# Optimization experiments

Measured on AMD Instinct MI355X. Metric: run time of the kernel, lower is better.

The kernel has to match this reference:

```python
import jax, jax.numpy as jnp
import numpy as np

N, E, D = 50000, 800000, 128
EPS = 1e-5


def _layernorm(x, g, b):
    m = jnp.mean(x, axis=-1, keepdims=True)
    v = jnp.mean((x - m) ** 2, axis=-1, keepdims=True)
    return (x - m) * jax.lax.rsqrt(v + EPS) * g + b


def setup_inputs() -> dict:
    key = jax.random.key(0)
    ks = jax.random.split(key, 8)
    x = jax.random.normal(ks[0], (N, D), dtype=jnp.float32)
    edge_index = jax.random.randint(ks[1], (2, E), 0, N, dtype=jnp.int64)
    edge_weights = jax.random.uniform(ks[2], (E,), dtype=jnp.float32)
    s = 1.0 / np.sqrt(D)
    W1 = jax.random.uniform(ks[3], (D, D), minval=-s, maxval=s, dtype=jnp.float32)
    b1 = jax.random.uniform(ks[4], (D,), minval=-s, maxval=s, dtype=jnp.float32)
    W2 = jax.random.uniform(ks[5], (D, D), minval=-s, maxval=s, dtype=jnp.float32)
    b2 = jax.random.uniform(ks[6], (D,), minval=-s, maxval=s, dtype=jnp.float32)
    g1 = jnp.ones((D,), jnp.float32); be1 = jnp.zeros((D,), jnp.float32)
    g2 = jnp.ones((D,), jnp.float32); be2 = jnp.zeros((D,), jnp.float32)
    return {"x": x, "edge_index": edge_index, "edge_weights": edge_weights,
            "W1": W1, "b1": b1, "g1": g1, "be1": be1,
            "W2": W2, "b2": b2, "g2": g2, "be2": be2}


def _layer(x, src, dst, ew, W, b, g, be):
    h = jax.nn.relu(x @ W + b)                      # [N, D]
    msg = ew[:, None] * h[src]                      # [E, D] gather
    h = h + jax.ops.segment_sum(msg, dst, num_segments=N)  # scatter-add (matches serial loop)
    return _layernorm(h, g, be)                     # dropout is identity at inference


def reference(x, edge_index, edge_weights, W1, b1, g1, be1, W2, b2, g2, be2):
    src, dst = edge_index[0], edge_index[1]
    x = _layer(x, src, dst, edge_weights, W1, b1, g1, be1)
    x = _layer(x, src, dst, edge_weights, W2, b2, g2, be2)
    return x
```

## Files before the change

### kernel.cpp

```cpp
#include <hip/hip_runtime.h>
#include <hip/hip_bf16.h>


#define D 128
#define SA 8192

typedef __attribute__((ext_vector_type(8))) short short8;
typedef __attribute__((ext_vector_type(4))) float f32x4;
typedef __attribute__((ext_vector_type(2))) unsigned int uint2v;
typedef __attribute__((ext_vector_type(4))) unsigned int uint4v;

__global__ __launch_bounds__(256) void k_prep(const float* __restrict__ W1,
                                              const float* __restrict__ W2,
                                              short* __restrict__ WT1,
                                              short* __restrict__ WT2,
                                              int* __restrict__ bhist, int nb) {
    int b = blockIdx.x;
    if (b < 128) {
        const float* W = (b < 64) ? W1 : W2;
        short* WT = (b < 64) ? WT1 : WT2;
        int i = (b & 63) * 256 + threadIdx.x;
        int k = i >> 7, nn = i & 127;
        WT[nn * 128 + k] = (short)__bfloat16_as_ushort(__float2bfloat16(W[i]));
    } else {
        for (int i = threadIdx.x; i < nb; i += 256) bhist[i] = 0;
    }
}

__global__ __launch_bounds__(1024) void k_bhist(const int* __restrict__ dst, int e,
                                                int n, int nb,
                                                int* __restrict__ bhist) {
    __shared__ int lh[784];
    int tid = threadIdx.x;
    for (int i = tid; i < nb; i += 1024) lh[i] = 0;
    __syncthreads();
    int i0 = blockIdx.x * SA;
#pragma unroll
    for (int k = 0; k < SA / 1024; ++k) {
        int i = i0 + k * 1024 + tid;
        if (i < e) {
            int d = dst[i];
            d = min(max(d, 0), n - 1);
            atomicAdd(&lh[d >> 6], 1);
        }
    }
    __syncthreads();
    for (int i = tid; i < nb; i += 1024)
        if (lh[i]) atomicAdd(&bhist[i], lh[i]);
}

__global__ __launch_bounds__(1024) void k_bscan(const int* __restrict__ bhist, int nb,
                                                int* __restrict__ boff,
                                                int* __restrict__ bcursor) {
    __shared__ int s[1024];
    int t = threadIdx.x;
    int v = (t < nb) ? bhist[t] : 0;
    s[t] = v;
    __syncthreads();
    for (int off = 1; off < 1024; off <<= 1) {
        int u = (t >= off) ? s[t - off] : 0;
        __syncthreads();
        s[t] += u;
        __syncthreads();
    }
    if (t < nb) {
        int ex = s[t] - v;
        boff[t] = ex;
        bcursor[t] = ex;
    }
}

__global__ __launch_bounds__(1024) void k_bfill(const int* __restrict__ src,
                                                const int* __restrict__ dst,
                                                const float* __restrict__ ew, int e,
                                                int n, int nb,
                                                int* __restrict__ bcursor,
                                                uint2v* __restrict__ csr_tmp) {
    __shared__ int lh[784];
    __shared__ int gbase[784];
    int tid = threadIdx.x;
    for (int i = tid; i < nb; i += 1024) lh[i] = 0;
    __syncthreads();
    int i0 = blockIdx.x * SA;
    int bkt[SA / 1024], pos[SA / 1024];
    unsigned pk[SA / 1024];
    float wv[SA / 1024];
#pragma unroll
    for (int k = 0; k < SA / 1024; ++k) {
        int i = i0 + k * 1024 + tid;
        bkt[k] = -1;
        if (i < e) {
            int d = dst[i];
            d = min(max(d, 0), n - 1);
            int s = src[i];
            s = min(max(s, 0), n - 1);
            int b = d >> 6;
            bkt[k] = b;
            pos[k] = atomicAdd(&lh[b], 1);
            pk[k] = (unsigned)s | ((unsigned)(d & 63) << 16);
            wv[k] = ew[i];
        }
    }
    __syncthreads();
    for (int i = tid; i < nb; i += 1024)
        gbase[i] = lh[i] ? atomicAdd(&bcursor[i], lh[i]) : 0;
    __syncthreads();
#pragma unroll
    for (int k = 0; k < SA / 1024; ++k) {
        if (bkt[k] >= 0) {
            int idx = gbase[bkt[k]] + pos[k];
            uint2v en;
            en.x = pk[k];
            en.y = __float_as_uint(wv[k]);
            csr_tmp[idx] = en;
        }
    }
}

#define STG 3072
__global__ __launch_bounds__(256) void k_bfinal(const uint2v* __restrict__ csr_tmp,
                                                const int* __restrict__ boff, int n,
                                                int e, int nb,
                                                int* __restrict__ row_ptr,
                                                uint2v* __restrict__ csr) {
    __shared__ uint2v stage[STG];
    __shared__ int dh[64], dcur[64], dscan[64];
    int b = blockIdx.x;
    int tid = threadIdx.x;
    int base = boff[b];
    int endo = (b + 1 < nb) ? boff[b + 1] : e;
    int cnt = endo - base;
    int ndst = min(64, n - b * 64);
    bool st = (cnt <= STG);
    if (tid < 64) { dh[tid] = 0; dcur[tid] = 0; }
    __syncthreads();
    for (int i = tid; i < cnt; i += 256) {
        uint2v en = csr_tmp[base + i];
        if (st) stage[i] = en;
        atomicAdd(&dh[(en.x >> 16) & 63], 1);
    }
    __syncthreads();
    if (tid < 64) {
        int v = dh[tid];
        int incl = v;
#pragma unroll
        for (int off = 1; off < 64; off <<= 1) {
            int u = __shfl_up(incl, off, 64);
            if (tid >= off) incl += u;
        }
        dscan[tid] = incl - v;
        if (tid < ndst) row_ptr[b * 64 + tid] = base + incl - v;
        if (b == nb - 1 && tid == 0) row_ptr[n] = e;
    }
    __syncthreads();
    for (int i = tid; i < cnt; i += 256) {
        uint2v en = st ? stage[i] : csr_tmp[base + i];
        int dlo = (en.x >> 16) & 63;
        int p = atomicAdd(&dcur[dlo], 1);
        csr[base + dscan[dlo] + p] = en;
    }
}

__device__ __forceinline__ short8 cvt8v(f32x4 lo, f32x4 hi) {
    short8 r;
    r[0] = (short)__bfloat16_as_ushort(__float2bfloat16(lo.x));
    r[1] = (short)__bfloat16_as_ushort(__float2bfloat16(lo.y));
    r[2] = (short)__bfloat16_as_ushort(__float2bfloat16(lo.z));
    r[3] = (short)__bfloat16_as_ushort(__float2bfloat16(lo.w));
    r[4] = (short)__bfloat16_as_ushort(__float2bfloat16(hi.x));
    r[5] = (short)__bfloat16_as_ushort(__float2bfloat16(hi.y));
    r[6] = (short)__bfloat16_as_ushort(__float2bfloat16(hi.z));
    r[7] = (short)__bfloat16_as_ushort(__float2bfloat16(hi.w));
    return r;
}

template <int F32IN>
__global__ __launch_bounds__(256) void k_gemm_mfma(const float* __restrict__ xf,
                                                   const short* __restrict__ xb,
                                                   const short* __restrict__ WT,
                                                   const float* __restrict__ bias,
                                                   ushort* __restrict__ hb, int n) {
    int lane = threadIdx.x & 63;
    int w = threadIdx.x >> 6;
    int ln = lane & 15, g = lane >> 4;
    int nt0 = w, nt1 = w + 4;
    short8 bfr0[4], bfr1[4];
#pragma unroll
    for (int kk = 0; kk < 4; ++kk) {
        bfr0[kk] = *(const short8*)(WT + (nt0 * 16 + ln) * 128 + kk * 32 + g * 8);
        bfr1[kk] = *(const short8*)(WT + (nt1 * 16 + ln) * 128 + kk * 32 + g * 8);
    }
    float bv0 = bias[nt0 * 16 + ln];
    float bv1 = bias[nt1 * 16 + ln];

    int ntile = n >> 4;
    int t = blockIdx.x;
    if (t >= ntile) return;

    f32x4 cf[8];
    short8 cb[4];
    auto LOADA = [&](int tt, f32x4* bf, short8* bb) {
        int row = tt * 16 + ln;
        if (F32IN) {
            const f32x4* p = (const f32x4*)(xf + (size_t)row * 128 + g * 8);
#pragma unroll
            for (int kk = 0; kk < 4; ++kk) {
                bf[kk * 2] = p[kk * 8];
                bf[kk * 2 + 1] = p[kk * 8 + 1];
            }
        } else {
            const short8* p = (const short8*)(xb + (size_t)row * 128 + g * 8);
#pragma unroll
            for (int kk = 0; kk < 4; ++kk) bb[kk] = p[kk * 4];
        }
    };
    LOADA(t, cf, cb);
    while (true) {
        int tn = t + (int)gridDim.x;
        f32x4 nf[8];
        short8 nb_[4];
        if (tn < ntile) LOADA(tn, nf, nb_);
        short8 a[4];
        if (F32IN) {
#pragma unroll
            for (int kk = 0; kk < 4; ++kk) a[kk] = cvt8v(cf[kk * 2], cf[kk * 2 + 1]);
        } else {
#pragma unroll
            for (int kk = 0; kk < 4; ++kk) a[kk] = cb[kk];
        }
        f32x4 acc0 = {}, acc1 = {};
#pragma unroll
        for (int kk = 0; kk < 4; ++kk) {
            acc0 = __builtin_amdgcn_mfma_f32_16x16x32_bf16(a[kk], bfr0[kk], acc0, 0, 0, 0);
            acc1 = __builtin_amdgcn_mfma_f32_16x16x32_bf16(a[kk], bfr1[kk], acc1, 0, 0, 0);
        }
        int r0 = t * 16 + g * 4;
#pragma unroll
        for (int r = 0; r < 4; ++r) {
            float v0 = fmaxf(acc0[r] + bv0, 0.0f);
            float v1 = fmaxf(acc1[r] + bv1, 0.0f);
            hb[(size_t)(r0 + r) * 128 + nt0 * 16 + ln] =
                __bfloat16_as_ushort(__float2bfloat16(v0));
            hb[(size_t)(r0 + r) * 128 + nt1 * 16 + ln] =
                __bfloat16_as_ushort(__float2bfloat16(v1));
        }
        if (tn >= ntile) break;
#pragma unroll
        for (int i = 0; i < 8; ++i) cf[i] = nf[i];
#pragma unroll
        for (int i = 0; i < 4; ++i) cb[i] = nb_[i];
        t = tn;
    }
}

__global__ __launch_bounds__(256) void k_aggln(const ushort* __restrict__ hb,
                                               const float* __restrict__ gamma,
                                               const float* __restrict__ beta,
                                               const int* __restrict__ row_ptr,
                                               const uint2v* __restrict__ csr,
                                               float* __restrict__ out,
                                               uint* __restrict__ xb_out,
                                               int n) {
    int wid = threadIdx.x >> 6;
    int lane = threadIdx.x & 63;
    int node = blockIdx.x * 4 + wid;
    if (node >= n) return;
    int sub = lane >> 4, c = lane & 15;
    const uint4v* hb4 = (const uint4v*)hb;

    float acc[8] = {0.f, 0.f, 0.f, 0.f, 0.f, 0.f, 0.f, 0.f};
    auto ACC8 = [&](uint4v r, float wgt) {
        acc[0] += wgt * __uint_as_float(r.x << 16);
        acc[1] += wgt * __uint_as_float(r.x & 0xffff0000u);
        acc[2] += wgt * __uint_as_float(r.y << 16);
        acc[3] += wgt * __uint_as_float(r.y & 0xffff0000u);
        acc[4] += wgt * __uint_as_float(r.z << 16);
        acc[5] += wgt * __uint_as_float(r.z & 0xffff0000u);
        acc[6] += wgt * __uint_as_float(r.w << 16);
        acc[7] += wgt * __uint_as_float(r.w & 0xffff0000u);
    };

    int beg = row_ptr[node], end = row_ptr[node + 1];
    int j = beg;
    for (; j + 16 <= end; j += 16) {
        uint2v e0 = csr[j + sub];
        uint2v e1 = csr[j + 4 + sub];
        uint2v e2 = csr[j + 8 + sub];
        uint2v e3 = csr[j + 12 + sub];
        uint4v r0 = hb4[(e0.x & 0xffffu) * 16 + c];
        uint4v r1 = hb4[(e1.x & 0xffffu) * 16 + c];
        uint4v r2 = hb4[(e2.x & 0xffffu) * 16 + c];
        uint4v r3 = hb4[(e3.x & 0xffffu) * 16 + c];
        ACC8(r0, __uint_as_float(e0.y));
        ACC8(r1, __uint_as_float(e1.y));
        ACC8(r2, __uint_as_float(e2.y));
        ACC8(r3, __uint_as_float(e3.y));
    }
    for (; j < end; j += 4) {
        int jj = j + sub;
        uint2v e = csr[jj < end ? jj : (end - 1)];
        float wgt = (jj < end) ? __uint_as_float(e.y) : 0.0f;
        uint idx = (jj < end) ? (e.x & 0xffffu) : (uint)node;
        uint4v r = hb4[idx * 16 + c];
        ACC8(r, wgt);
    }
#pragma unroll
    for (int i = 0; i < 8; ++i) {
        acc[i] += __shfl_xor(acc[i], 16, 64);
        acc[i] += __shfl_xor(acc[i], 32, 64);
    }
    {
        uint4v s = hb4[(uint)node * 16 + c];
        ACC8(s, 1.0f);
    }
    float sum = acc[0] + acc[1] + acc[2] + acc[3] + acc[4] + acc[5] + acc[6] + acc[7];
#pragma unroll
    for (int m = 1; m < 16; m <<= 1) sum += __shfl_xor(sum, m, 64);
    float mean = sum * (1.0f / 128.0f);
    float d0 = acc[0] - mean, d1 = acc[1] - mean, d2 = acc[2] - mean, d3 = acc[3] - mean;
    float d4 = acc[4] - mean, d5 = acc[5] - mean, d6 = acc[6] - mean, d7 = acc[7] - mean;
    float ss = d0 * d0 + d1 * d1 + d2 * d2 + d3 * d3 + d4 * d4 + d5 * d5 + d6 * d6 + d7 * d7;
#pragma unroll
    for (int m = 1; m < 16; m <<= 1) ss += __shfl_xor(ss, m, 64);
    float rstd = rsqrtf(ss * (1.0f / 128.0f) + 1e-5f);
    f32x4 gA = ((const f32x4*)gamma)[c * 2], gB = ((const f32x4*)gamma)[c * 2 + 1];
    f32x4 bA = ((const f32x4*)beta)[c * 2], bB = ((const f32x4*)beta)[c * 2 + 1];
    f32x4 oA, oB;
    oA.x = d0 * rstd * gA.x + bA.x;
    oA.y = d1 * rstd * gA.y + bA.y;
    oA.z = d2 * rstd * gA.z + bA.z;
    oA.w = d3 * rstd * gA.w + bA.w;
    oB.x = d4 * rstd * gB.x + bB.x;
    oB.y = d5 * rstd * gB.y + bB.y;
    oB.z = d6 * rstd * gB.z + bB.z;
    oB.w = d7 * rstd * gB.w + bB.w;
    if (sub == 0) {
        if (out) {
            f32x4* po = (f32x4*)(out + (size_t)node * 128 + c * 8);
            po[0] = oA;
            po[1] = oB;
        }
        if (xb_out) {
            uint4v u;
            u.x = (uint)__bfloat16_as_ushort(__float2bfloat16(oA.x)) |
                  ((uint)__bfloat16_as_ushort(__float2bfloat16(oA.y)) << 16);
            u.y = (uint)__bfloat16_as_ushort(__float2bfloat16(oA.z)) |
                  ((uint)__bfloat16_as_ushort(__float2bfloat16(oA.w)) << 16);
            u.z = (uint)__bfloat16_as_ushort(__float2bfloat16(oB.x)) |
                  ((uint)__bfloat16_as_ushort(__float2bfloat16(oB.y)) << 16);
            u.w = (uint)__bfloat16_as_ushort(__float2bfloat16(oB.z)) |
                  ((uint)__bfloat16_as_ushort(__float2bfloat16(oB.w)) << 16);
            ((uint4v*)xb_out)[node * 16 + c] = u;
        }
    }
}

extern "C" void kernel_launch(void* const* d_in, const int* in_sizes, int n_in,
                              void* d_out, int out_size, void* d_ws, size_t ws_size,
                              hipStream_t stream) {
    const float* x   = (const float*)d_in[0];
    const int*  eidx = (const int*)d_in[1];
    const float* ew  = (const float*)d_in[2];
    const float* W1  = (const float*)d_in[3];
    const float* b1  = (const float*)d_in[4];
    const float* g1  = (const float*)d_in[5];
    const float* be1 = (const float*)d_in[6];
    const float* W2  = (const float*)d_in[7];
    const float* b2  = (const float*)d_in[8];
    const float* g2  = (const float*)d_in[9];
    const float* be2 = (const float*)d_in[10];
    int n = in_sizes[0] / D;
    int e = in_sizes[2];
    const int* srcp = eidx;
    const int* dstp = eidx + e;

    char* ws = (char*)d_ws;
    size_t off = 0;
    auto alloc = [&](size_t bytes) {
        void* p = ws + off;
        off += (bytes + 255) & ~(size_t)255;
        return p;
    };
    ushort* hb      = (ushort*)alloc((size_t)n * D * sizeof(ushort));
    uint*   xb      = (uint*)alloc((size_t)n * (D / 2) * sizeof(uint));
    int*    row_ptr = (int*)alloc((size_t)(n + 1) * sizeof(int));
    int*    bhist   = (int*)alloc(1024 * sizeof(int));
    int*    boff    = (int*)alloc(1024 * sizeof(int));
    int*    bcursor = (int*)alloc(1024 * sizeof(int));
    short*  WT1     = (short*)alloc(128 * 128 * sizeof(short));
    short*  WT2     = (short*)alloc(128 * 128 * sizeof(short));
    uint2v* csr_tmp = (uint2v*)alloc((size_t)e * sizeof(uint2v));
    uint2v* csr     = (uint2v*)alloc((size_t)e * sizeof(uint2v));

    int nb = (n + 63) >> 6;
    int nblk = (e + SA - 1) / SA;

    k_prep<<<129, 256, 0, stream>>>(W1, W2, WT1, WT2, bhist, nb);
    k_bhist<<<nblk, 1024, 0, stream>>>(dstp, e, n, nb, bhist);
    k_bscan<<<1, 1024, 0, stream>>>(bhist, nb, boff, bcursor);
    k_bfill<<<nblk, 1024, 0, stream>>>(srcp, dstp, ew, e, n, nb, bcursor, csr_tmp);
    k_bfinal<<<nb, 256, 0, stream>>>(csr_tmp, boff, n, e, nb, row_ptr, csr);

    k_gemm_mfma<1><<<512, 256, 0, stream>>>(x, nullptr, WT1, b1, hb, n);
    k_aggln<<<(n + 3) / 4, 256, 0, stream>>>(hb, g1, be1, row_ptr, csr,
                                             nullptr, xb, n);
    k_gemm_mfma<0><<<512, 256, 0, stream>>>(nullptr, (const short*)xb, WT2, b2, hb, n);
    k_aggln<<<(n + 3) / 4, 256, 0, stream>>>(hb, g2, be2, row_ptr, csr,
                                             (float*)d_out, nullptr, n);
}
```

Measured before the change: 142.8 us.

## Merge prep/histogram and final-CSR/GEMM1 launches, pack CSR edges into 32 bits

Folds weight transposition into the histogram kernel, which now writes per-block partial histograms that the scan kernel sums. This drops the separate zeroing pass and the global atomics. The final CSR bucketing kernel and the first GEMM now run as one launch with disjoint block ranges, so they can overlap. CSR entries are packed into 32 bits (16-bit source index plus bf16 weight), which halves edge-list traffic in aggregation but rounds edge weights to bf16. The 16-bit source field only holds indices below 65536, which N=50000 satisfies.

```diff
diff --git a/kernel.cpp b/kernel.cpp
--- a/kernel.cpp
+++ b/kernel.cpp
@@ -10,51 +10,51 @@
 typedef __attribute__((ext_vector_type(2))) unsigned int uint2v;
 typedef __attribute__((ext_vector_type(4))) unsigned int uint4v;
 
-__global__ __launch_bounds__(256) void k_prep(const float* __restrict__ W1,
-                                              const float* __restrict__ W2,
-                                              short* __restrict__ WT1,
-                                              short* __restrict__ WT2,
-                                              int* __restrict__ bhist, int nb) {
-    int b = blockIdx.x;
-    if (b < 128) {
-        const float* W = (b < 64) ? W1 : W2;
-        short* WT = (b < 64) ? WT1 : WT2;
-        int i = (b & 63) * 256 + threadIdx.x;
-        int k = i >> 7, nn = i & 127;
-        WT[nn * 128 + k] = (short)__bfloat16_as_ushort(__float2bfloat16(W[i]));
+__global__ __launch_bounds__(1024) void k_hist_prep(
+        const int* __restrict__ dst, int e, int n, int nb, int nblk,
+        int* __restrict__ part,
+        const float* __restrict__ W1, const float* __restrict__ W2,
+        short* __restrict__ WT1, short* __restrict__ WT2) {
+    __shared__ int lh[784];
+    int b = blockIdx.x, tid = threadIdx.x;
+    if (b < nblk) {
+        for (int i = tid; i < nb; i += 1024) lh[i] = 0;
+        __syncthreads();
+        int i0 = b * SA;
+#pragma unroll
+        for (int k = 0; k < SA / 1024; ++k) {
+            int i = i0 + k * 1024 + tid;
+            if (i < e) {
+                int d = dst[i];
+                d = min(max(d, 0), n - 1);
+                atomicAdd(&lh[d >> 6], 1);
+            }
+        }
+        __syncthreads();
+        for (int i = tid; i < nb; i += 1024) part[b * nb + i] = lh[i];
     } else {
-        for (int i = threadIdx.x; i < nb; i += 256) bhist[i] = 0;
-    }
-}
-
-__global__ __launch_bounds__(1024) void k_bhist(const int* __restrict__ dst, int e,
-                                                int n, int nb,
-                                                int* __restrict__ bhist) {
-    __shared__ int lh[784];
-    int tid = threadIdx.x;
-    for (int i = tid; i < nb; i += 1024) lh[i] = 0;
-    __syncthreads();
-    int i0 = blockIdx.x * SA;
-#pragma unroll
-    for (int k = 0; k < SA / 1024; ++k) {
-        int i = i0 + k * 1024 + tid;
-        if (i < e) {
-            int d = dst[i];
-            d = min(max(d, 0), n - 1);
-            atomicAdd(&lh[d >> 6], 1);
-        }
-    }
-    __syncthreads();
-    for (int i = tid; i < nb; i += 1024)
-        if (lh[i]) atomicAdd(&bhist[i], lh[i]);
-}
-
-__global__ __launch_bounds__(1024) void k_bscan(const int* __restrict__ bhist, int nb,
+        int q = b - nblk;
+        int i = q * 1024 + tid;
+        if (i < 16384) {
+            int k = i >> 7, nn = i & 127;
+            WT1[nn * 128 + k] = (short)__bfloat16_as_ushort(__float2bfloat16(W1[i]));
+        } else {
+            int j = i - 16384;
+            int k = j >> 7, nn = j & 127;
+            WT2[nn * 128 + k] = (short)__bfloat16_as_ushort(__float2bfloat16(W2[j]));
+        }
+    }
+}
+
+__global__ __launch_bounds__(1024) void k_bscan(const int* __restrict__ part,
+                                                int nb, int nblk,
                                                 int* __restrict__ boff,
                                                 int* __restrict__ bcursor) {
     __shared__ int s[1024];
     int t = threadIdx.x;
-    int v = (t < nb) ? bhist[t] : 0;
+    int v = 0;
+    if (t < nb)
+        for (int blk = 0; blk < nblk; ++blk) v += part[blk * nb + t];
     s[t] = v;
     __syncthreads();
     for (int off = 1; off < 1024; off <<= 1) {
@@ -117,50 +117,6 @@
     }
 }
 
-#define STG 3072
-__global__ __launch_bounds__(256) void k_bfinal(const uint2v* __restrict__ csr_tmp,
-                                                const int* __restrict__ boff, int n,
-                                                int e, int nb,
-                                                int* __restrict__ row_ptr,
-                                                uint2v* __restrict__ csr) {
-    __shared__ uint2v stage[STG];
-    __shared__ int dh[64], dcur[64], dscan[64];
-    int b = blockIdx.x;
-    int tid = threadIdx.x;
-    int base = boff[b];
-    int endo = (b + 1 < nb) ? boff[b + 1] : e;
-    int cnt = endo - base;
-    int ndst = min(64, n - b * 64);
-    bool st = (cnt <= STG);
-    if (tid < 64) { dh[tid] = 0; dcur[tid] = 0; }
-    __syncthreads();
-    for (int i = tid; i < cnt; i += 256) {
-        uint2v en = csr_tmp[base + i];
-        if (st) stage[i] = en;
-        atomicAdd(&dh[(en.x >> 16) & 63], 1);
-    }
-    __syncthreads();
-    if (tid < 64) {
-        int v = dh[tid];
-        int incl = v;
-#pragma unroll
-        for (int off = 1; off < 64; off <<= 1) {
-            int u = __shfl_up(incl, off, 64);
-            if (tid >= off) incl += u;
-        }
-        dscan[tid] = incl - v;
-        if (tid < ndst) row_ptr[b * 64 + tid] = base + incl - v;
-        if (b == nb - 1 && tid == 0) row_ptr[n] = e;
-    }
-    __syncthreads();
-    for (int i = tid; i < cnt; i += 256) {
-        uint2v en = st ? stage[i] : csr_tmp[base + i];
-        int dlo = (en.x >> 16) & 63;
-        int p = atomicAdd(&dcur[dlo], 1);
-        csr[base + dscan[dlo] + p] = en;
-    }
-}
-
 __device__ __forceinline__ short8 cvt8v(f32x4 lo, f32x4 hi) {
     short8 r;
     r[0] = (short)__bfloat16_as_ushort(__float2bfloat16(lo.x));
@@ -175,11 +131,12 @@
 }
 
 template <int F32IN>
-__global__ __launch_bounds__(256) void k_gemm_mfma(const float* __restrict__ xf,
-                                                   const short* __restrict__ xb,
-                                                   const short* __restrict__ WT,
-                                                   const float* __restrict__ bias,
-                                                   ushort* __restrict__ hb, int n) {
+__device__ __forceinline__ void gemm_body(int bid, int nblocks,
+                                          const float* __restrict__ xf,
+                                          const short* __restrict__ xb,
+                                          const short* __restrict__ WT,
+                                          const float* __restrict__ bias,
+                                          ushort* __restrict__ hb, int n) {
     int lane = threadIdx.x & 63;
     int w = threadIdx.x >> 6;
     int ln = lane & 15, g = lane >> 4;
@@ -194,7 +151,7 @@
     float bv1 = bias[nt1 * 16 + ln];
 
     int ntile = n >> 4;
-    int t = blockIdx.x;
+    int t = bid;
     if (t >= ntile) return;
 
     f32x4 cf[8];
@@ -216,7 +173,7 @@
     };
     LOADA(t, cf, cb);
     while (true) {
-        int tn = t + (int)gridDim.x;
+        int tn = t + nblocks;
         f32x4 nf[8];
         short8 nb_[4];
         if (tn < ntile) LOADA(tn, nf, nb_);
@@ -253,11 +210,74 @@
     }
 }
 
+#define STG 3072
+__global__ __launch_bounds__(256) void k_final_gemm1(
+        const uint2v* __restrict__ csr_tmp, const int* __restrict__ boff,
+        int n, int e, int nb,
+        int* __restrict__ row_ptr, uint* __restrict__ csr4,
+        const float* __restrict__ xf, const short* __restrict__ WT1,
+        const float* __restrict__ bias1, ushort* __restrict__ hb,
+        int gemm_blocks) {
+    __shared__ uint2v stage[STG];
+    __shared__ int dh[64], dcur[64], dscan[64];
+    int b = blockIdx.x;
+    int tid = threadIdx.x;
+    if (b >= nb) {
+        gemm_body<1>(b - nb, gemm_blocks, xf, nullptr, WT1, bias1, hb, n);
+        return;
+    }
+    int base = boff[b];
+    int endo = (b + 1 < nb) ? boff[b + 1] : e;
+    int cnt = endo - base;
+    int ndst = min(64, n - b * 64);
+    bool st = (cnt <= STG);
+    if (tid < 64) { dh[tid] = 0; dcur[tid] = 0; }
+    __syncthreads();
+    for (int i = tid; i < cnt; i += 256) {
+        uint2v en = csr_tmp[base + i];
+        if (st) stage[i] = en;
+        atomicAdd(&dh[(en.x >> 16) & 63], 1);
+    }
+    __syncthreads();
+    if (tid < 64) {
+        int v = dh[tid];
+        int incl = v;
+#pragma unroll
+        for (int off = 1; off < 64; off <<= 1) {
+            int u = __shfl_up(incl, off, 64);
+            if (tid >= off) incl += u;
+        }
+        dscan[tid] = incl - v;
+        if (tid < ndst) row_ptr[b * 64 + tid] = base + incl - v;
+        if (b == nb - 1 && tid == 0) row_ptr[n] = e;
+    }
+    __syncthreads();
+    for (int i = tid; i < cnt; i += 256) {
+        uint2v en = st ? stage[i] : csr_tmp[base + i];
+        int dlo = (en.x >> 16) & 63;
+        int p = atomicAdd(&dcur[dlo], 1);
+        uint packed = (en.x & 0xffffu) |
+                      ((uint)__bfloat16_as_ushort(
+                           __float2bfloat16(__uint_as_float(en.y))) << 16);
+        csr4[base + dscan[dlo] + p] = packed;
+    }
+}
+
+template <int F32IN>
+__global__ __launch_bounds__(256) void k_gemm(const float* __restrict__ xf,
+                                              const short* __restrict__ xb,
+                                              const short* __restrict__ WT,
+                                              const float* __restrict__ bias,
+                                              ushort* __restrict__ hb, int n,
+                                              int nblocks) {
+    gemm_body<F32IN>(blockIdx.x, nblocks, xf, xb, WT, bias, hb, n);
+}
+
 __global__ __launch_bounds__(256) void k_aggln(const ushort* __restrict__ hb,
                                                const float* __restrict__ gamma,
                                                const float* __restrict__ beta,
                                                const int* __restrict__ row_ptr,
-                                               const uint2v* __restrict__ csr,
+                                               const uint* __restrict__ csru,
                                                float* __restrict__ out,
                                                uint* __restrict__ xb_out,
                                                int n) {
@@ -283,24 +303,24 @@
     int beg = row_ptr[node], end = row_ptr[node + 1];
     int j = beg;
     for (; j + 16 <= end; j += 16) {
-        uint2v e0 = csr[j + sub];
-        uint2v e1 = csr[j + 4 + sub];
-        uint2v e2 = csr[j + 8 + sub];
-        uint2v e3 = csr[j + 12 + sub];
-        uint4v r0 = hb4[(e0.x & 0xffffu) * 16 + c];
-        uint4v r1 = hb4[(e1.x & 0xffffu) * 16 + c];
-        uint4v r2 = hb4[(e2.x & 0xffffu) * 16 + c];
-        uint4v r3 = hb4[(e3.x & 0xffffu) * 16 + c];
-        ACC8(r0, __uint_as_float(e0.y));
-        ACC8(r1, __uint_as_float(e1.y));
-        ACC8(r2, __uint_as_float(e2.y));
-        ACC8(r3, __uint_as_float(e3.y));
+        uint e0 = csru[j + sub];
+        uint e1 = csru[j + 4 + sub];
+        uint e2 = csru[j + 8 + sub];
+        uint e3 = csru[j + 12 + sub];
+        uint4v r0 = hb4[(e0 & 0xffffu) * 16 + c];
+        uint4v r1 = hb4[(e1 & 0xffffu) * 16 + c];
+        uint4v r2 = hb4[(e2 & 0xffffu) * 16 + c];
+        uint4v r3 = hb4[(e3 & 0xffffu) * 16 + c];
+        ACC8(r0, __uint_as_float(e0 & 0xffff0000u));
+        ACC8(r1, __uint_as_float(e1 & 0xffff0000u));
+        ACC8(r2, __uint_as_float(e2 & 0xffff0000u));
+        ACC8(r3, __uint_as_float(e3 & 0xffff0000u));
     }
     for (; j < end; j += 4) {
         int jj = j + sub;
-        uint2v e = csr[jj < end ? jj : (end - 1)];
-        float wgt = (jj < end) ? __uint_as_float(e.y) : 0.0f;
-        uint idx = (jj < end) ? (e.x & 0xffffu) : (uint)node;
+        uint ee = csru[jj < end ? jj : (end - 1)];
+        float wgt = (jj < end) ? __uint_as_float(ee & 0xffff0000u) : 0.0f;
+        uint idx = (jj < end) ? (ee & 0xffffu) : (uint)node;
         uint4v r = hb4[idx * 16 + c];
         ACC8(r, wgt);
     }
@@ -384,27 +404,27 @@
     ushort* hb      = (ushort*)alloc((size_t)n * D * sizeof(ushort));
     uint*   xb      = (uint*)alloc((size_t)n * (D / 2) * sizeof(uint));
     int*    row_ptr = (int*)alloc((size_t)(n + 1) * sizeof(int));
-    int*    bhist   = (int*)alloc(1024 * sizeof(int));
     int*    boff    = (int*)alloc(1024 * sizeof(int));
     int*    bcursor = (int*)alloc(1024 * sizeof(int));
     short*  WT1     = (short*)alloc(128 * 128 * sizeof(short));
     short*  WT2     = (short*)alloc(128 * 128 * sizeof(short));
     uint2v* csr_tmp = (uint2v*)alloc((size_t)e * sizeof(uint2v));
-    uint2v* csr     = (uint2v*)alloc((size_t)e * sizeof(uint2v));
+    uint*   csr4    = (uint*)alloc((size_t)e * sizeof(uint));
 
     int nb = (n + 63) >> 6;
     int nblk = (e + SA - 1) / SA;
-
-    k_prep<<<129, 256, 0, stream>>>(W1, W2, WT1, WT2, bhist, nb);
-    k_bhist<<<nblk, 1024, 0, stream>>>(dstp, e, n, nb, bhist);
-    k_bscan<<<1, 1024, 0, stream>>>(bhist, nb, boff, bcursor);
+    int* part = (int*)alloc((size_t)nblk * nb * sizeof(int));
+
+    k_hist_prep<<<nblk + 32, 1024, 0, stream>>>(dstp, e, n, nb, nblk, part,
+                                                W1, W2, WT1, WT2);
+    k_bscan<<<1, 1024, 0, stream>>>(part, nb, nblk, boff, bcursor);
     k_bfill<<<nblk, 1024, 0, stream>>>(srcp, dstp, ew, e, n, nb, bcursor, csr_tmp);
-    k_bfinal<<<nb, 256, 0, stream>>>(csr_tmp, boff, n, e, nb, row_ptr, csr);
-
-    k_gemm_mfma<1><<<512, 256, 0, stream>>>(x, nullptr, WT1, b1, hb, n);
-    k_aggln<<<(n + 3) / 4, 256, 0, stream>>>(hb, g1, be1, row_ptr, csr,
+
+    k_final_gemm1<<<nb + 512, 256, 0, stream>>>(csr_tmp, boff, n, e, nb, row_ptr,
+                                                csr4, x, WT1, b1, hb, 512);
+    k_aggln<<<(n + 3) / 4, 256, 0, stream>>>(hb, g1, be1, row_ptr, csr4,
                                              nullptr, xb, n);
-    k_gemm_mfma<0><<<512, 256, 0, stream>>>(nullptr, (const short*)xb, WT2, b2, hb, n);
-    k_aggln<<<(n + 3) / 4, 256, 0, stream>>>(hb, g2, be2, row_ptr, csr,
+    k_gemm<0><<<512, 256, 0, stream>>>(nullptr, (const short*)xb, WT2, b2, hb, n, 512);
+    k_aggln<<<(n + 3) / 4, 256, 0, stream>>>(hb, g2, be2, row_ptr, csr4,
                                              (float*)d_out, nullptr, n);
 }
```

Measured after the change: 167.9 us. +17.6%, slower.
